# Kernel tuning notes

Hardware: AMD Instinct MI355X
Metric: run time of the kernel (lower is better)

The kernel has to match this reference:

```python
import jax, jax.numpy as jnp
import numpy as np

B, T, C = 2, 2048, 2048
N, K, H = 16, 4, 128      # heads, kv heads, head dim
G = N // K                # query groups per kv head
ROPE_THETA = 10000.0
N_LAYERS = 24
SOFTCAP = 50.0


def _sine_table(features, length, max_timescale):
    fraction = jnp.arange(0, features, 2, dtype=jnp.float32) / features
    timescale = max_timescale ** fraction  # min_timescale = 1.0
    sinusoid = jnp.einsum('i,j->ij', jnp.arange(length, dtype=jnp.float32),
                          1.0 / timescale, precision=jax.lax.Precision.HIGHEST)
    sinusoid = jnp.concatenate([sinusoid, sinusoid], axis=-1)  # (length, features)
    return jnp.sin(sinusoid), jnp.cos(sinusoid)


def _rotate_half(x):
    x1, x2 = jnp.split(x, 2, axis=-1)
    return jnp.concatenate([-x2, x1], axis=-1)


def setup_inputs() -> dict:
    key = jax.random.key(0)
    kx, kq, kk, kv, ko = jax.random.split(key, 5)
    init_std = np.sqrt(2.0 / (5.0 * C)).astype(np.float32)
    wang_std = np.float32(2.0 / N_LAYERS / np.sqrt(N * H))
    return {
        'x': jax.random.normal(kx, (B, T, C), dtype=jnp.float32),
        'q_kernel': jax.random.normal(kq, (C, N * H), dtype=jnp.float32) * init_std,
        'k_kernel': jax.random.normal(kk, (C, K * H), dtype=jnp.float32) * init_std,
        'v_kernel': jax.random.normal(kv, (C, K * H), dtype=jnp.float32) * init_std,
        'out_kernel': jax.random.normal(ko, (N * H, C), dtype=jnp.float32) * wang_std,
    }


def reference(x, q_kernel, k_kernel, v_kernel, out_kernel):
    q = jnp.dot(x, q_kernel).reshape(B, T, K, G, H)
    k = jnp.dot(x, k_kernel).reshape(B, T, K, H)
    v = jnp.dot(x, v_kernel).reshape(B, T, K, H)

    # RoPE (note original passes cos into the `sin` slot and vice versa by name,
    # but the computation uses cos with identity part and sin with rotate_half).
    sin, cos = _sine_table(H, T, ROPE_THETA)
    qcos = cos[None, :, None, None, :]  # (1,T,1,1,H)
    qsin = sin[None, :, None, None, :]
    kcos = cos[None, :, None, :]        # (1,T,1,H)
    ksin = sin[None, :, None, :]
    q = q * qcos + _rotate_half(q) * qsin
    k = k * kcos + _rotate_half(k) * ksin

    scale = jax.lax.rsqrt(jnp.float32(H))
    logits = jnp.einsum('btkgh,bskh->bkgts', q * scale, k)  # (B,K,G,T,S)
    logits = jnp.tanh(logits / SOFTCAP) * SOFTCAP
    causal = jnp.tril(jnp.ones((T, T), dtype=jnp.bool_))
    neg = jnp.asarray(-0.7 * jnp.finfo(logits.dtype).max, dtype=logits.dtype)
    logits = jnp.where(causal[None, None, None, :, :], logits, neg)
    probs = jax.nn.softmax(logits.astype(jnp.float32), axis=-1).astype(logits.dtype)
    encoded = jnp.einsum('bkgts,bskh->btkgh', probs, v)
    encoded = encoded.reshape(B, T, N * H)
    return jnp.dot(encoded, out_kernel)
```

## Files before the change

### kernel.cpp

```cpp
#include <hip/hip_runtime.h>
#include <stdint.h>

typedef unsigned short u16;
typedef __bf16 bf16x8 __attribute__((ext_vector_type(8)));
typedef __bf16 bf16x4 __attribute__((ext_vector_type(4)));
typedef float f32x4 __attribute__((ext_vector_type(4)));

#define T_SEQ 2048
#define KVH 4

__device__ __forceinline__ u16 f2b(float f) {
  uint32_t u = __builtin_bit_cast(uint32_t, f);
  u += 0x7FFFu + ((u >> 16) & 1u);
  return (u16)(u >> 16);
}
__device__ __forceinline__ float b2f(u16 h) {
  uint32_t u = ((uint32_t)h) << 16;
  return __builtin_bit_cast(float, u);
}

__device__ __forceinline__ void gload16(const void* g, void* l) {
  __builtin_amdgcn_global_load_lds((const __attribute__((address_space(1))) void*)g,
                                   (__attribute__((address_space(3))) void*)l, 16, 0, 0);
}

__global__ void k_prep(const float* __restrict__ x, u16* __restrict__ x_bf,
                       const float* __restrict__ wq, const float* __restrict__ wk,
                       const float* __restrict__ wv, const float* __restrict__ wo,
                       u16* __restrict__ wqkvt, u16* __restrict__ wot) {
  const int z = blockIdx.z;
  const int tid = threadIdx.y * 32 + threadIdx.x;
  if (z == 3) {
    const int base = (blockIdx.y * 64 + blockIdx.x) * 256 + tid;
#pragma unroll
    for (int rep = 0; rep < 2; ++rep) {
      const int i = base + rep * 1048576;
      float4 v = reinterpret_cast<const float4*>(x)[i];
      ushort4 o;
      o.x = f2b(v.x); o.y = f2b(v.y); o.z = f2b(v.z); o.w = f2b(v.w);
      reinterpret_cast<ushort4*>(x_bf)[i] = o;
    }
    return;
  }
  __shared__ float tile[32][33];
  int bx = blockIdx.x;
  const float* in;
  u16* out;
  int Cc;
  if (z == 0)      { in = wq; out = wqkvt;              Cc = 2048; }
  else if (z == 1) { in = wo; out = wot;                Cc = 2048; }
  else {
    if (bx < 16)      { in = wk; out = wqkvt + 2048 * 2048; Cc = 512; }
    else if (bx < 32) { in = wv; out = wqkvt + 2560 * 2048; Cc = 512; bx -= 16; }
    else return;
  }
  const int R = 2048;
  const int c0 = bx * 32, r0 = blockIdx.y * 32;
  const int tx = threadIdx.x, ty = threadIdx.y;
  for (int i = ty; i < 32; i += 8) tile[i][tx] = in[(size_t)(r0 + i) * Cc + c0 + tx];
  __syncthreads();
  for (int i = ty; i < 32; i += 8) out[(size_t)(c0 + i) * R + r0 + tx] = f2b(tile[tx][i]);
}

template <int OUT_BF16>
__global__ __launch_bounds__(256, 3) void k_gemm(const u16* __restrict__ A,
                                                 const u16* __restrict__ Bt,
                                                 void* __restrict__ Cp,
                                                 int M, int N, int Kd,
                                                 int lda, int ldb, int ldc) {
  __align__(16) __shared__ u16 As[128 * 64];
  __align__(16) __shared__ u16 Bs[128 * 64];
  const int tid = threadIdx.x;
  const int wid = tid >> 6, lane = tid & 63;
  const int lg = lane >> 4, lm = lane & 15;
  const int nwg = gridDim.x * gridDim.y;
  int f = blockIdx.y * gridDim.x + blockIdx.x;
  f = (f & 7) * (nwg >> 3) + (f >> 3);
  const int bm = f % gridDim.x, bn = f / gridDim.x;
  const int wr = wid >> 1, wc = wid & 1;

  const u16* ap[4];
  const u16* bp[4];
#pragma unroll
  for (int i = 0; i < 4; ++i) {
    const int g = tid + i * 256;
    const int row = g >> 3, u = g & 7;
    ap[i] = A + (size_t)(bm * 128 + row) * lda + ((u ^ (row & 7)) * 8);
    bp[i] = Bt + (size_t)(bn * 128 + row) * ldb + ((u ^ (row & 7)) * 8);
  }

  const int swzl = lm & 7;
  int aoff[4][2], boff[4][2];
#pragma unroll
  for (int i = 0; i < 4; ++i)
#pragma unroll
    for (int kk = 0; kk < 2; ++kk) {
      aoff[i][kk] = (wr * 64 + i * 16 + lm) * 64 + (((kk * 4 + lg) ^ swzl) * 8);
      boff[i][kk] = (wc * 64 + i * 16 + lm) * 64 + (((kk * 4 + lg) ^ swzl) * 8);
    }

  const f32x4 z4 = {0.f, 0.f, 0.f, 0.f};
  f32x4 acc[4][4];
#pragma unroll
  for (int i = 0; i < 4; ++i)
#pragma unroll
    for (int j = 0; j < 4; ++j) acc[i][j] = z4;

  const int nk = Kd >> 6;
  for (int kb = 0; kb < nk; ++kb) {
#pragma unroll
    for (int i = 0; i < 4; ++i) {
      const int g = tid + i * 256;
      gload16(ap[i], As + g * 8);
      gload16(bp[i], Bs + g * 8);
      ap[i] += 64;
      bp[i] += 64;
    }
    __syncthreads();
#pragma unroll
    for (int kk = 0; kk < 2; ++kk) {
      bf16x8 af[4], bfr[4];
#pragma unroll
      for (int i = 0; i < 4; ++i) {
        af[i] = *(const bf16x8*)(As + aoff[i][kk]);
        bfr[i] = *(const bf16x8*)(Bs + boff[i][kk]);
      }
#pragma unroll
      for (int i = 0; i < 4; ++i)
#pragma unroll
        for (int j = 0; j < 4; ++j)
          acc[i][j] = __builtin_amdgcn_mfma_f32_16x16x32_bf16(af[i], bfr[j], acc[i][j], 0, 0, 0);
    }
    __syncthreads();
  }

#pragma unroll
  for (int i = 0; i < 4; ++i) {
    const int row = bm * 128 + wr * 64 + i * 16 + lg * 4;
#pragma unroll
    for (int j = 0; j < 4; ++j) {
      const int col = bn * 128 + wc * 64 + j * 16 + lm;
#pragma unroll
      for (int r = 0; r < 4; ++r) {
        const float v = acc[i][j][r];
        if (OUT_BF16)
          ((u16*)Cp)[(size_t)(row + r) * ldc + col] = __builtin_bit_cast(u16, (__bf16)v);
        else
          ((float*)Cp)[(size_t)(row + r) * ldc + col] = v;
      }
    }
  }
}

__global__ void k_rope_v(const u16* __restrict__ qkv, u16* __restrict__ kbf,
                         u16* __restrict__ vt) {
  __shared__ u16 tile[32][33];
  const int bid = blockIdx.x;
  const int tid = threadIdx.x;
  if (bid < 4096) {
    const int idx = bid * 256 + tid;
    const int j = idx & 63;
    const int kh = (idx >> 6) & 3;
    const int m = idx >> 8;
    const int t = m & (T_SEQ - 1);
    const int b = m >> 11;
    const float inv = __expf((float)j * -0.14391157f);
    const float ang = (float)t * inv;
    float s, c;
    __sincosf(ang, &s, &c);
    const u16* row = qkv + (size_t)m * 3072 + 2048 + kh * 128;
    const float x1 = b2f(row[j]), x2 = b2f(row[j + 64]);
    u16* orow = kbf + ((size_t)(b * KVH + kh) * T_SEQ + t) * 128;
    orow[j] = f2b(x1 * c - x2 * s);
    orow[j + 64] = f2b(x2 * c + x1 * s);
  } else {
    const int vb = bid - 4096;
    const int t0 = (vb & 63) * 32, h0 = ((vb >> 6) & 3) * 32, bk = vb >> 8;
    const int b = bk >> 2, kh = bk & 3;
    const int tx = tid & 31, ty = tid >> 5;
    for (int i = ty; i < 32; i += 8)
      tile[i][tx] = qkv[(size_t)(b * T_SEQ + t0 + i) * 3072 + 2560 + kh * 128 + h0 + tx];
    __syncthreads();
    for (int i = ty; i < 32; i += 8)
      vt[(size_t)bk * (128 * T_SEQ) + (size_t)(h0 + i) * T_SEQ + t0 + tx] = tile[tx][i];
  }
}

__global__ __launch_bounds__(256, 2) void k_attn(const u16* __restrict__ qkv,
                                                 const u16* __restrict__ kbf,
                                                 const u16* __restrict__ vt,
                                                 u16* __restrict__ enc) {
  __shared__ __align__(16) u16 smem[36864];
  u16* const Ks0 = smem;
  u16* const Vs0 = smem + 16384;

  const int n = blockIdx.y, b = blockIdx.z;
  const int qt = (b == 0) ? (15 - blockIdx.x) : blockIdx.x;
  const int kh = n >> 2;
  const int tid = threadIdx.x;
  const int wid = tid >> 6;
  const int lane = tid & 63;
  const int lg = lane >> 4;
  const int lm = lane & 15;
  const int q0w = qt * 128 + wid * 32;
  u16* const Pl = smem + 32768 + wid * 1024;

  bf16x8 qfA[4], qfB[4];
  {
    const u16* qa = qkv + (size_t)(b * T_SEQ + q0w + lm) * 3072 + n * 128 + lg * 8;
    const u16* qb_ = qa + 16 * 3072;
    bf16x8 ra[4], rb[4];
#pragma unroll
    for (int c = 0; c < 4; ++c) {
      ra[c] = *(const bf16x8*)(qa + c * 32);
      rb[c] = *(const bf16x8*)(qb_ + c * 32);
    }
    const float scale = 0.08838834764831845f;
    const float tA = (float)(q0w + lm), tB = (float)(q0w + 16 + lm);
#pragma unroll
    for (int c = 0; c < 2; ++c) {
#pragma unroll
      for (int k = 0; k < 8; ++k) {
        const float inv = __expf((float)(c * 32 + lg * 8 + k) * -0.14391157f);
        float sA, cA, sB, cB;
        __sincosf(tA * inv, &sA, &cA);
        __sincosf(tB * inv, &sB, &cB);
        const float a1 = (float)ra[c][k], a2 = (float)ra[c + 2][k];
        const float b1 = (float)rb[c][k], b2 = (float)rb[c + 2][k];
        qfA[c][k]     = (__bf16)((a1 * cA - a2 * sA) * scale);
        qfA[c + 2][k] = (__bf16)((a2 * cA + a1 * sA) * scale);
        qfB[c][k]     = (__bf16)((b1 * cB - b2 * sB) * scale);
        qfB[c + 2][k] = (__bf16)((b2 * cB + b1 * sB) * scale);
      }
    }
  }
  const u16* const kg = kbf + (size_t)(b * KVH + kh) * T_SEQ * 128;
  const u16* const vg = vt + (size_t)(b * KVH + kh) * 128 * T_SEQ;

  const int swz = lm & 7;
  int koff[4], voff[2], poff[4];
#pragma unroll
  for (int c = 0; c < 4; ++c) koff[c] = lm * 128 + (((c * 4 + lg) ^ swz) * 8);
#pragma unroll
  for (int ks = 0; ks < 2; ++ks) voff[ks] = lm * 64 + (((ks * 4 + lg) ^ swz) * 8);
#pragma unroll
  for (int st = 0; st < 4; ++st)
    poff[st] = lm * 64 + (((st * 2 + (lg >> 1)) ^ swz) * 8) + (lg & 1) * 4;

  const f32x4 z4 = {0.f, 0.f, 0.f, 0.f};
  f32x4 accA[8], accB[8];
#pragma unroll
  for (int h = 0; h < 8; ++h) { accA[h] = z4; accB[h] = z4; }
  float lA = 0.f, lB = 0.f;

  const int ntiles = 2 * qt + 2;

  auto STAGE = [&](int buf, int kb2) {
    const int kv2 = kb2 * 64;
    const u16* ksrc = kg + (size_t)kv2 * 128;
    u16* kdst = Ks0 + buf * 8192;
    u16* vdst = Vs0 + buf * 8192;
#pragma unroll
    for (int i = 0; i < 4; ++i) {
      const int g = tid + i * 256;
      const int row = g >> 4, u = g & 15;
      gload16(ksrc + row * 128 + ((u ^ (row & 7)) * 8), kdst + g * 8);
    }
#pragma unroll
    for (int i = 0; i < 4; ++i) {
      const int g = tid + i * 256;
      const int row = g >> 3, u = g & 7;
      gload16(vg + (size_t)row * T_SEQ + kv2 + ((u ^ (row & 7)) * 8), vdst + g * 8);
    }
  };

  auto tile_pc = [&](f32x4* sa, float* p, float& lsum, int tg, bool needMask, int kv) {
#pragma unroll
    for (int st = 0; st < 4; ++st)
#pragma unroll
      for (int r = 0; r < 4; ++r) p[st * 4 + r] = sa[st][r];
#pragma unroll
    for (int i = 0; i < 16; ++i) {
      const float e = __builtin_amdgcn_exp2f(p[i] * 0.05770780163555853f);
      p[i] = __builtin_amdgcn_exp2f(-144.269504088896f * __builtin_amdgcn_rcpf(e + 1.f));
    }
    if (needMask) {
#pragma unroll
      for (int i = 0; i < 16; ++i) {
        const int sg = kv + (i >> 2) * 16 + lg * 4 + (i & 3);
        if (sg > tg) p[i] = 0.f;
      }
    }
#pragma unroll
    for (int i = 0; i < 16; ++i) lsum += p[i];
  };
  auto tile_pw = [&](const float* p) {
#pragma unroll
    for (int st = 0; st < 4; ++st) {
      bf16x4 w4;
#pragma unroll
      for (int r = 0; r < 4; ++r) w4[r] = (__bf16)p[st * 4 + r];
      *(bf16x4*)(Pl + poff[st]) = w4;
    }
  };

  STAGE(0, 0);
  asm volatile("s_waitcnt vmcnt(0)" ::: "memory");
  __syncthreads();

  for (int kb = 0; kb < ntiles; ++kb) {
    const int cur = kb & 1;
    if (kb + 1 < ntiles) STAGE(cur ^ 1, kb + 1);
    const int kv = kb * 64;
    if (kv <= q0w + 31) {
      const u16* KsC = Ks0 + cur * 8192;
      const u16* VsC = Vs0 + cur * 8192;

      f32x4 saA[4] = {z4, z4, z4, z4};
      f32x4 saB[4] = {z4, z4, z4, z4};
      __builtin_amdgcn_s_setprio(1);
#pragma unroll
      for (int st = 0; st < 4; ++st) {
#pragma unroll
        for (int c = 0; c < 4; ++c) {
          const bf16x8 kf = *(const bf16x8*)(KsC + st * 2048 + koff[c]);
          saA[st] = __builtin_amdgcn_mfma_f32_16x16x32_bf16(kf, qfA[c], saA[st], 0, 0, 0);
          saB[st] = __builtin_amdgcn_mfma_f32_16x16x32_bf16(kf, qfB[c], saB[st], 0, 0, 0);
        }
      }
      __builtin_amdgcn_s_setprio(0);

      float pA[16], pB[16];
      tile_pc(saA, pA, lA, q0w + lm, kv + 63 > q0w, kv);
      tile_pw(pA);
      tile_pc(saB, pB, lB, q0w + 16 + lm, kv + 63 > q0w + 16, kv);
      asm volatile("s_waitcnt lgkmcnt(0)" ::: "memory");
      bf16x8 pfA[2], pfB[2];
#pragma unroll
      for (int ks = 0; ks < 2; ++ks) pfA[ks] = *(const bf16x8*)(Pl + voff[ks]);
      tile_pw(pB);
      asm volatile("s_waitcnt lgkmcnt(0)" ::: "memory");
#pragma unroll
      for (int ks = 0; ks < 2; ++ks) pfB[ks] = *(const bf16x8*)(Pl + voff[ks]);

      __builtin_amdgcn_s_setprio(1);
#pragma unroll
      for (int h = 0; h < 8; ++h) {
#pragma unroll
        for (int ks = 0; ks < 2; ++ks) {
          const bf16x8 vf = *(const bf16x8*)(VsC + h * 1024 + voff[ks]);
          accA[h] = __builtin_amdgcn_mfma_f32_16x16x32_bf16(pfA[ks], vf, accA[h], 0, 0, 0);
          accB[h] = __builtin_amdgcn_mfma_f32_16x16x32_bf16(pfB[ks], vf, accB[h], 0, 0, 0);
        }
      }
      __builtin_amdgcn_s_setprio(0);
    }
    asm volatile("s_waitcnt vmcnt(0)" ::: "memory");
    __syncthreads();
  }

  lA += __shfl_xor(lA, 16); lA += __shfl_xor(lA, 32);
  lB += __shfl_xor(lB, 16); lB += __shfl_xor(lB, 32);
  float liA[4], liB[4];
#pragma unroll
  for (int r = 0; r < 4; ++r) {
    liA[r] = 1.f / __shfl(lA, lg * 4 + r);
    liB[r] = 1.f / __shfl(lB, lg * 4 + r);
  }
#pragma unroll
  for (int h = 0; h < 8; ++h) {
#pragma unroll
    for (int r = 0; r < 4; ++r) {
      const size_t colo = n * 128 + h * 16 + lm;
      enc[(size_t)(b * T_SEQ + q0w + lg * 4 + r) * 2048 + colo] =
          __builtin_bit_cast(u16, (__bf16)(accA[h][r] * liA[r]));
      enc[(size_t)(b * T_SEQ + q0w + 16 + lg * 4 + r) * 2048 + colo] =
          __builtin_bit_cast(u16, (__bf16)(accB[h][r] * liB[r]));
    }
  }
}

extern "C" void kernel_launch(void* const* d_in, const int* in_sizes, int n_in,
                              void* d_out, int out_size, void* d_ws, size_t ws_size,
                              hipStream_t stream) {
  const float* x  = (const float*)d_in[0];
  const float* wq = (const float*)d_in[1];
  const float* wk = (const float*)d_in[2];
  const float* wv = (const float*)d_in[3];
  const float* wo = (const float*)d_in[4];

  char* ws = (char*)d_ws;
  u16* x_bf  = (u16*)(ws);
  u16* wqkvt = (u16*)(ws + 16777216);
  u16* wot   = (u16*)(ws + 29360128);
  u16* qkv   = (u16*)(ws + 37748736);
  u16* enc   = (u16*)(ws + 62914560);
  u16* k_bf  = (u16*)(ws + 79691776);
  u16* vt    = (u16*)(ws + 83886080);
  if (ws_size < 88080384) return;
  (void)in_sizes; (void)n_in; (void)out_size;

  k_prep<<<dim3(64, 64, 4), dim3(32, 8), 0, stream>>>(x, x_bf, wq, wk, wv, wo, wqkvt, wot);
  k_gemm<1><<<dim3(32, 24), dim3(256), 0, stream>>>(x_bf, wqkvt, qkv,
                                                    4096, 3072, 2048, 2048, 2048, 3072);
  k_rope_v<<<dim3(6144), dim3(256), 0, stream>>>(qkv, k_bf, vt);
  k_attn<<<dim3(16, 16, 2), dim3(256), 0, stream>>>(qkv, k_bf, vt, enc);
  k_gemm<0><<<dim3(32, 16), dim3(256), 0, stream>>>(enc, wot, d_out,
                                                    4096, 2048, 2048, 2048, 2048, 2048);
}
```

Baseline: 187.4 us.

## Halve attention block size and load V fragments directly from global memory

The attention kernel now runs 128-thread blocks covering 64 query rows, doubling the grid, and uses a new query-tile ordering that balances causal work across heads and batches. Only K is staged in shared memory through the double buffer. Each wave now reads its V fragments straight from global memory into registers every tile, which removes V shared-memory staging and cuts LDS size. In exchange, V reuse across waves is lost, global V traffic per block rises, register pressure grows, and global load latency now sits inside the compute loop without prefetch.

```diff
diff --git a/kernel.cpp b/kernel.cpp
--- a/kernel.cpp
+++ b/kernel.cpp
@@ -186,24 +186,23 @@
   }
 }
 
-__global__ __launch_bounds__(256, 2) void k_attn(const u16* __restrict__ qkv,
+__global__ __launch_bounds__(128, 2) void k_attn(const u16* __restrict__ qkv,
                                                  const u16* __restrict__ kbf,
                                                  const u16* __restrict__ vt,
                                                  u16* __restrict__ enc) {
-  __shared__ __align__(16) u16 smem[36864];
-  u16* const Ks0 = smem;
-  u16* const Vs0 = smem + 16384;
+  __shared__ __align__(16) u16 smem[18432];
 
   const int n = blockIdx.y, b = blockIdx.z;
-  const int qt = (b == 0) ? (15 - blockIdx.x) : blockIdx.x;
+  const int bx = blockIdx.x;
+  const int qt = (b == 0) ? ((n < 8) ? bx : 31 - bx) : ((n < 8) ? 31 - bx : bx);
   const int kh = n >> 2;
   const int tid = threadIdx.x;
   const int wid = tid >> 6;
   const int lane = tid & 63;
   const int lg = lane >> 4;
   const int lm = lane & 15;
-  const int q0w = qt * 128 + wid * 32;
-  u16* const Pl = smem + 32768 + wid * 1024;
+  const int q0w = qt * 64 + wid * 32;
+  u16* const Pl = smem + 16384 + wid * 1024;
 
   bf16x8 qfA[4], qfB[4];
   {
@@ -253,24 +252,16 @@
   for (int h = 0; h < 8; ++h) { accA[h] = z4; accB[h] = z4; }
   float lA = 0.f, lB = 0.f;
 
-  const int ntiles = 2 * qt + 2;
-
-  auto STAGE = [&](int buf, int kb2) {
-    const int kv2 = kb2 * 64;
-    const u16* ksrc = kg + (size_t)kv2 * 128;
-    u16* kdst = Ks0 + buf * 8192;
-    u16* vdst = Vs0 + buf * 8192;
-#pragma unroll
-    for (int i = 0; i < 4; ++i) {
-      const int g = tid + i * 256;
+  const int ntiles = qt + 1;
+
+  auto STAGEK = [&](int buf, int kb2) {
+    const u16* ksrc = kg + (size_t)kb2 * 64 * 128;
+    u16* kdst = smem + buf * 8192;
+#pragma unroll
+    for (int i = 0; i < 8; ++i) {
+      const int g = tid + i * 128;
       const int row = g >> 4, u = g & 15;
       gload16(ksrc + row * 128 + ((u ^ (row & 7)) * 8), kdst + g * 8);
-    }
-#pragma unroll
-    for (int i = 0; i < 4; ++i) {
-      const int g = tid + i * 256;
-      const int row = g >> 3, u = g & 7;
-      gload16(vg + (size_t)row * T_SEQ + kv2 + ((u ^ (row & 7)) * 8), vdst + g * 8);
     }
   };
 
@@ -304,17 +295,26 @@
     }
   };
 
-  STAGE(0, 0);
+  STAGEK(0, 0);
   asm volatile("s_waitcnt vmcnt(0)" ::: "memory");
   __syncthreads();
 
   for (int kb = 0; kb < ntiles; ++kb) {
     const int cur = kb & 1;
-    if (kb + 1 < ntiles) STAGE(cur ^ 1, kb + 1);
+    if (kb + 1 < ntiles) STAGEK(cur ^ 1, kb + 1);
     const int kv = kb * 64;
     if (kv <= q0w + 31) {
-      const u16* KsC = Ks0 + cur * 8192;
-      const u16* VsC = Vs0 + cur * 8192;
+      const u16* KsC = smem + cur * 8192;
+
+      bf16x8 vf[8][2];
+      {
+        const u16* vrow = vg + (size_t)lm * T_SEQ + kv + lg * 8;
+#pragma unroll
+        for (int h = 0; h < 8; ++h)
+#pragma unroll
+          for (int ks = 0; ks < 2; ++ks)
+            vf[h][ks] = *(const bf16x8*)(vrow + (size_t)(h * 16) * T_SEQ + ks * 32);
+      }
 
       f32x4 saA[4] = {z4, z4, z4, z4};
       f32x4 saB[4] = {z4, z4, z4, z4};
@@ -348,9 +348,8 @@
       for (int h = 0; h < 8; ++h) {
 #pragma unroll
         for (int ks = 0; ks < 2; ++ks) {
-          const bf16x8 vf = *(const bf16x8*)(VsC + h * 1024 + voff[ks]);
-          accA[h] = __builtin_amdgcn_mfma_f32_16x16x32_bf16(pfA[ks], vf, accA[h], 0, 0, 0);
-          accB[h] = __builtin_amdgcn_mfma_f32_16x16x32_bf16(pfB[ks], vf, accB[h], 0, 0, 0);
+          accA[h] = __builtin_amdgcn_mfma_f32_16x16x32_bf16(pfA[ks], vf[h][ks], accA[h], 0, 0, 0);
+          accB[h] = __builtin_amdgcn_mfma_f32_16x16x32_bf16(pfB[ks], vf[h][ks], accB[h], 0, 0, 0);
         }
       }
       __builtin_amdgcn_s_setprio(0);
@@ -404,7 +403,7 @@
   k_gemm<1><<<dim3(32, 24), dim3(256), 0, stream>>>(x_bf, wqkvt, qkv,
                                                     4096, 3072, 2048, 2048, 2048, 3072);
   k_rope_v<<<dim3(6144), dim3(256), 0, stream>>>(qkv, k_bf, vt);
-  k_attn<<<dim3(16, 16, 2), dim3(256), 0, stream>>>(qkv, k_bf, vt, enc);
+  k_attn<<<dim3(32, 16, 2), dim3(128), 0, stream>>>(qkv, k_bf, vt, enc);
   k_gemm<0><<<dim3(32, 16), dim3(256), 0, stream>>>(enc, wot, d_out,
                                                     4096, 2048, 2048, 2048, 2048, 2048);
 }
```

Measured after the change: 209.4 us. 1.12x slower.

## Fuse K RoPE and V transpose into QKV GEMM epilogue

Applied to the files above, without the earlier changes.

The QKV GEMM epilogue now stages K and V output tiles in shared memory. It applies RoPE to K and writes it to the per-head K buffer, and writes V transposed directly to vt. This removes the separate k_rope_v kernel launch and its global reread of the K/V part of qkv. The cost is extra epilogue work and shared-memory traffic in the K/V column blocks.

```diff
diff --git a/kernel.cpp b/kernel.cpp
--- a/kernel.cpp
+++ b/kernel.cpp
@@ -62,14 +62,17 @@
   for (int i = ty; i < 32; i += 8) out[(size_t)(c0 + i) * R + r0 + tx] = f2b(tile[tx][i]);
 }
 
-template <int OUT_BF16>
+template <int MODE>
 __global__ __launch_bounds__(256, 3) void k_gemm(const u16* __restrict__ A,
                                                  const u16* __restrict__ Bt,
                                                  void* __restrict__ Cp,
+                                                 u16* __restrict__ kbf,
+                                                 u16* __restrict__ vt,
                                                  int M, int N, int Kd,
                                                  int lda, int ldb, int ldc) {
-  __align__(16) __shared__ u16 As[128 * 64];
-  __align__(16) __shared__ u16 Bs[128 * 64];
+  __shared__ __align__(16) u16 sh[16384];
+  u16* const As = sh;
+  u16* const Bs = sh + 8192;
   const int tid = threadIdx.x;
   const int wid = tid >> 6, lane = tid & 63;
   const int lg = lane >> 4, lm = lane & 15;
@@ -134,6 +137,60 @@
     __syncthreads();
   }
 
+  if (MODE == 1 && bn >= 16) {
+    const bool isK = bn < 20;
+    const int kh = isK ? (bn - 16) : (bn - 20);
+#pragma unroll
+    for (int i = 0; i < 4; ++i)
+#pragma unroll
+      for (int j = 0; j < 4; ++j)
+#pragma unroll
+        for (int r = 0; r < 4; ++r) {
+          const int lr = wr * 64 + i * 16 + lg * 4 + r;
+          const int lc = wc * 64 + j * 16 + lm;
+          sh[isK ? (lr * 128 + lc) : (lc * 128 + lr)] =
+              __builtin_bit_cast(u16, (__bf16)acc[i][j][r]);
+        }
+    __syncthreads();
+    const int b = bm >> 4;
+    const int tbase = (bm & 15) * 128;
+    if (isK) {
+      const int tr = tid >> 1;
+      const int j0 = (tid & 1) * 32;
+      const int t = tbase + tr;
+      u16* orow = kbf + ((size_t)(b * KVH + kh) * T_SEQ + t) * 128;
+      u16 xlo[32], xhi[32], olo[32], ohi[32];
+#pragma unroll
+      for (int q = 0; q < 4; ++q) {
+        *(uint4*)(xlo + q * 8) = *(const uint4*)(sh + tr * 128 + j0 + q * 8);
+        *(uint4*)(xhi + q * 8) = *(const uint4*)(sh + tr * 128 + 64 + j0 + q * 8);
+      }
+#pragma unroll
+      for (int jj = 0; jj < 32; ++jj) {
+        const int j = j0 + jj;
+        const float x1 = b2f(xlo[jj]), x2 = b2f(xhi[jj]);
+        const float inv = __expf((float)j * -0.14391157f);
+        float s, c;
+        __sincosf((float)t * inv, &s, &c);
+        olo[jj] = f2b(x1 * c - x2 * s);
+        ohi[jj] = f2b(x2 * c + x1 * s);
+      }
+#pragma unroll
+      for (int q = 0; q < 4; ++q) {
+        *(uint4*)(orow + j0 + q * 8) = *(const uint4*)(olo + q * 8);
+        *(uint4*)(orow + 64 + j0 + q * 8) = *(const uint4*)(ohi + q * 8);
+      }
+    } else {
+      const int h = tid >> 1;
+      const int t0 = (tid & 1) * 64;
+      u16* vrow = vt + ((size_t)(b * KVH + kh) * 128 + h) * T_SEQ + tbase + t0;
+#pragma unroll
+      for (int q = 0; q < 8; ++q)
+        *(uint4*)(vrow + q * 8) = *(const uint4*)(sh + h * 128 + t0 + q * 8);
+    }
+    return;
+  }
+
 #pragma unroll
   for (int i = 0; i < 4; ++i) {
     const int row = bm * 128 + wr * 64 + i * 16 + lg * 4;
@@ -143,46 +200,12 @@
 #pragma unroll
       for (int r = 0; r < 4; ++r) {
         const float v = acc[i][j][r];
-        if (OUT_BF16)
+        if (MODE)
           ((u16*)Cp)[(size_t)(row + r) * ldc + col] = __builtin_bit_cast(u16, (__bf16)v);
         else
           ((float*)Cp)[(size_t)(row + r) * ldc + col] = v;
       }
     }
-  }
-}
-
-__global__ void k_rope_v(const u16* __restrict__ qkv, u16* __restrict__ kbf,
-                         u16* __restrict__ vt) {
-  __shared__ u16 tile[32][33];
-  const int bid = blockIdx.x;
-  const int tid = threadIdx.x;
-  if (bid < 4096) {
-    const int idx = bid * 256 + tid;
-    const int j = idx & 63;
-    const int kh = (idx >> 6) & 3;
-    const int m = idx >> 8;
-    const int t = m & (T_SEQ - 1);
-    const int b = m >> 11;
-    const float inv = __expf((float)j * -0.14391157f);
-    const float ang = (float)t * inv;
-    float s, c;
-    __sincosf(ang, &s, &c);
-    const u16* row = qkv + (size_t)m * 3072 + 2048 + kh * 128;
-    const float x1 = b2f(row[j]), x2 = b2f(row[j + 64]);
-    u16* orow = kbf + ((size_t)(b * KVH + kh) * T_SEQ + t) * 128;
-    orow[j] = f2b(x1 * c - x2 * s);
-    orow[j + 64] = f2b(x2 * c + x1 * s);
-  } else {
-    const int vb = bid - 4096;
-    const int t0 = (vb & 63) * 32, h0 = ((vb >> 6) & 3) * 32, bk = vb >> 8;
-    const int b = bk >> 2, kh = bk & 3;
-    const int tx = tid & 31, ty = tid >> 5;
-    for (int i = ty; i < 32; i += 8)
-      tile[i][tx] = qkv[(size_t)(b * T_SEQ + t0 + i) * 3072 + 2560 + kh * 128 + h0 + tx];
-    __syncthreads();
-    for (int i = ty; i < 32; i += 8)
-      vt[(size_t)bk * (128 * T_SEQ) + (size_t)(h0 + i) * T_SEQ + t0 + tx] = tile[tx][i];
   }
 }
 
@@ -401,10 +424,9 @@
   (void)in_sizes; (void)n_in; (void)out_size;
 
   k_prep<<<dim3(64, 64, 4), dim3(32, 8), 0, stream>>>(x, x_bf, wq, wk, wv, wo, wqkvt, wot);
-  k_gemm<1><<<dim3(32, 24), dim3(256), 0, stream>>>(x_bf, wqkvt, qkv,
+  k_gemm<1><<<dim3(32, 24), dim3(256), 0, stream>>>(x_bf, wqkvt, qkv, k_bf, vt,
                                                     4096, 3072, 2048, 2048, 2048, 3072);
-  k_rope_v<<<dim3(6144), dim3(256), 0, stream>>>(qkv, k_bf, vt);
   k_attn<<<dim3(16, 16, 2), dim3(256), 0, stream>>>(qkv, k_bf, vt, enc);
-  k_gemm<0><<<dim3(32, 16), dim3(256), 0, stream>>>(enc, wot, d_out,
+  k_gemm<0><<<dim3(32, 16), dim3(256), 0, stream>>>(enc, wot, d_out, nullptr, nullptr,
                                                     4096, 2048, 2048, 2048, 2048, 2048);
 }
```

After: 193.6 us. +3.3%, slower.
